# Performance work log

Hardware: AMD Instinct MI355X
Metric: run time of the kernel (lower is better)

Reference implementation:

```python
import jax, jax.numpy as jnp
import numpy as np

D_MODEL = 256
NUM_ENTRIES = 256 * 256


def _build_tables(op_fn):
    idx = np.arange(NUM_ENTRIES)
    a = idx >> 8
    b = idx & 255
    W1 = np.zeros((2 * D_MODEL, NUM_ENTRIES), dtype=np.float32)
    W1[a, idx] = 1.0
    W1[D_MODEL + b, idx] = 1.0
    res = op_fn(a, b) & 255
    W2 = np.zeros((NUM_ENTRIES, D_MODEL), dtype=np.float32)
    W2[idx, res] = 1.0
    return jnp.asarray(W1), jnp.asarray(W2)


def setup_inputs() -> dict:
    key = jax.random.key(0)
    k1, k2 = jax.random.split(key)
    a_emb = jax.random.normal(k1, (4, D_MODEL), dtype=jnp.float32)
    b_emb = jax.random.normal(k2, (4, D_MODEL), dtype=jnp.float32)
    # op='xor' table (op is a string selector in the original; fixed here)
    W1, W2 = _build_tables(np.bitwise_xor)
    return {"a_emb": a_emb, "b_emb": b_emb, "W1": W1, "W2": W2}


def reference(a_emb, b_emb, W1, W2):
    # x: [4, 512] = concat of the two byte embeddings per byte position
    x = jnp.concatenate([a_emb, b_emb], axis=-1)
    scores = x @ W1                                  # [4, 65536]
    weights = jax.nn.softmax((scores - 1.5) * 10.0, axis=-1)
    result = weights @ W2                            # [4, 256]
    return result
```

## Files before the change

### kernel.cpp

```cpp
#include <hip/hip_runtime.h>
#include <math.h>


__global__ __launch_bounds__(1024) void BitwiseOps_62380105007334_kernel(
    const float* __restrict__ a_emb,
    const float* __restrict__ b_emb,
    float* __restrict__ out)
{
    const int r    = blockIdx.x;
    const int tid  = threadIdx.x;
    const int lane = tid & 63;
    const int wave = tid >> 6;

    __shared__ float ea[256];
    __shared__ float eb[256];
    __shared__ float wred[16];
    __shared__ float scal[3];
    __shared__ float part[1024];

    float v = -1e30f;
    if (tid < 256)      v = a_emb[r * 256 + tid];
    else if (tid < 512) v = b_emb[r * 256 + (tid - 256)];

    float m = v;
    #pragma unroll
    for (int off = 32; off; off >>= 1) m = fmaxf(m, __shfl_xor(m, off, 64));
    if (lane == 0) wred[wave] = m;
    __syncthreads();
    if (tid == 0) {
        scal[0] = fmaxf(fmaxf(wred[0], wred[1]), fmaxf(wred[2], wred[3]));
        scal[1] = fmaxf(fmaxf(wred[4], wred[5]), fmaxf(wred[6], wred[7]));
    }
    __syncthreads();

    float e = 0.0f;
    if (tid < 512) {
        const float mm = (tid < 256) ? scal[0] : scal[1];
        e = expf(10.0f * (v - mm));
        if (tid < 256) ea[tid] = e;
        else           eb[tid - 256] = e;
    }
    float s = e;
    #pragma unroll
    for (int off = 32; off; off >>= 1) s += __shfl_xor(s, off, 64);
    if (lane == 0) wred[wave] = s;
    __syncthreads();
    if (tid == 0) {
        const float sa = wred[0] + wred[1] + wred[2] + wred[3];
        const float sb = wred[4] + wred[5] + wred[6] + wred[7];
        scal[2] = 1.0f / (sa * sb);
    }
    __syncthreads();

    const int c = tid & 255;
    const int p = tid >> 8;
    const int abase = p * 64;
    float acc = 0.0f;
    #pragma unroll 8
    for (int i = 0; i < 64; ++i) {
        const int a = abase + i;
        acc += ea[a] * eb[a ^ c];
    }
    part[tid] = acc;
    __syncthreads();

    if (tid < 256) {
        const float res = (part[tid] + part[tid + 256] + part[tid + 512] + part[tid + 768])
                          * scal[2];
        out[r * 256 + tid] = res;
    }
}

extern "C" void kernel_launch(void* const* d_in, const int* in_sizes, int n_in,
                              void* d_out, int out_size, void* d_ws, size_t ws_size,
                              hipStream_t stream) {
    const float* a_emb = (const float*)d_in[0];
    const float* b_emb = (const float*)d_in[1];
    float* out = (float*)d_out;
    BitwiseOps_62380105007334_kernel<<<4, 1024, 0, stream>>>(a_emb, b_emb, out);
}
```

Baseline: 9.263 us.

## Compute XOR-convolution softmax with Walsh-Hadamard transforms in a single wavefront

Replaces the O(256^2) shared-memory XOR convolution with forward Walsh-Hadamard transforms of the exponentiated embeddings, a pointwise product, and an inverse transform, all done with wave shuffles. The block shrinks to one 64-thread wave, removing LDS buffers and block-wide barriers. The max-subtraction step is dropped and the normalizer comes from the DC coefficient, which removes the reductions but risks fp32 overflow for large embedding values.

```diff
diff --git a/kernel.cpp b/kernel.cpp
--- a/kernel.cpp
+++ b/kernel.cpp
@@ -1,74 +1,53 @@
 #include <hip/hip_runtime.h>
-#include <math.h>
 
 
-__global__ __launch_bounds__(1024) void BitwiseOps_62380105007334_kernel(
+__device__ __forceinline__ void wht256(float v[4], int lane) {
+    float t0 = v[0] + v[1], t1 = v[0] - v[1];
+    float t2 = v[2] + v[3], t3 = v[2] - v[3];
+    v[0] = t0 + t2; v[1] = t1 + t3;
+    v[2] = t0 - t2; v[3] = t1 - t3;
+    #pragma unroll
+    for (int m = 1; m <= 32; m <<= 1) {
+        const float s = (lane & m) ? -1.0f : 1.0f;
+        #pragma unroll
+        for (int j = 0; j < 4; ++j) {
+            const float t = __shfl_xor(v[j], m, 64);
+            v[j] = fmaf(s, v[j], t);
+        }
+    }
+}
+
+__global__ __launch_bounds__(64) void BitwiseOps_62380105007334_kernel(
     const float* __restrict__ a_emb,
     const float* __restrict__ b_emb,
     float* __restrict__ out)
 {
     const int r    = blockIdx.x;
-    const int tid  = threadIdx.x;
-    const int lane = tid & 63;
-    const int wave = tid >> 6;
+    const int lane = threadIdx.x;
 
-    __shared__ float ea[256];
-    __shared__ float eb[256];
-    __shared__ float wred[16];
-    __shared__ float scal[3];
-    __shared__ float part[1024];
+    const float4 av = *reinterpret_cast<const float4*>(a_emb + r * 256 + lane * 4);
+    const float4 bv = *reinterpret_cast<const float4*>(b_emb + r * 256 + lane * 4);
 
-    float v = -1e30f;
-    if (tid < 256)      v = a_emb[r * 256 + tid];
-    else if (tid < 512) v = b_emb[r * 256 + (tid - 256)];
+    float fa[4] = { __expf(10.0f * av.x), __expf(10.0f * av.y),
+                    __expf(10.0f * av.z), __expf(10.0f * av.w) };
+    float fb[4] = { __expf(10.0f * bv.x), __expf(10.0f * bv.y),
+                    __expf(10.0f * bv.z), __expf(10.0f * bv.w) };
 
-    float m = v;
+    wht256(fa, lane);
+    wht256(fb, lane);
+
+    float p[4];
     #pragma unroll
-    for (int off = 32; off; off >>= 1) m = fmaxf(m, __shfl_xor(m, off, 64));
-    if (lane == 0) wred[wave] = m;
-    __syncthreads();
-    if (tid == 0) {
-        scal[0] = fmaxf(fmaxf(wred[0], wred[1]), fmaxf(wred[2], wred[3]));
-        scal[1] = fmaxf(fmaxf(wred[4], wred[5]), fmaxf(wred[6], wred[7]));
-    }
-    __syncthreads();
+    for (int j = 0; j < 4; ++j) p[j] = fa[j] * fb[j];
 
-    float e = 0.0f;
-    if (tid < 512) {
-        const float mm = (tid < 256) ? scal[0] : scal[1];
-        e = expf(10.0f * (v - mm));
-        if (tid < 256) ea[tid] = e;
-        else           eb[tid - 256] = e;
-    }
-    float s = e;
-    #pragma unroll
-    for (int off = 32; off; off >>= 1) s += __shfl_xor(s, off, 64);
-    if (lane == 0) wred[wave] = s;
-    __syncthreads();
-    if (tid == 0) {
-        const float sa = wred[0] + wred[1] + wred[2] + wred[3];
-        const float sb = wred[4] + wred[5] + wred[6] + wred[7];
-        scal[2] = 1.0f / (sa * sb);
-    }
-    __syncthreads();
+    const float p0 = __shfl(p[0], 0, 64);
 
-    const int c = tid & 255;
-    const int p = tid >> 8;
-    const int abase = p * 64;
-    float acc = 0.0f;
-    #pragma unroll 8
-    for (int i = 0; i < 64; ++i) {
-        const int a = abase + i;
-        acc += ea[a] * eb[a ^ c];
-    }
-    part[tid] = acc;
-    __syncthreads();
+    wht256(p, lane);
 
-    if (tid < 256) {
-        const float res = (part[tid] + part[tid + 256] + part[tid + 512] + part[tid + 768])
-                          * scal[2];
-        out[r * 256 + tid] = res;
-    }
+    const float inv = 1.0f / (256.0f * p0);
+    float4 o;
+    o.x = p[0] * inv; o.y = p[1] * inv; o.z = p[2] * inv; o.w = p[3] * inv;
+    *reinterpret_cast<float4*>(out + r * 256 + lane * 4) = o;
 }
 
 extern "C" void kernel_launch(void* const* d_in, const int* in_sizes, int n_in,
@@ -77,5 +56,5 @@
     const float* a_emb = (const float*)d_in[0];
     const float* b_emb = (const float*)d_in[1];
     float* out = (float*)d_out;
-    BitwiseOps_62380105007334_kernel<<<4, 1024, 0, stream>>>(a_emb, b_emb, out);
+    BitwiseOps_62380105007334_kernel<<<4, 64, 0, stream>>>(a_emb, b_emb, out);
 }
```

Result: slower. 9.716 us (+4.9%).
